# Performance work log

Measured on AMD Instinct MI355X. Metric: run time of the kernel, lower is better.

## Reference

```python
import jax, jax.numpy as jnp
import numpy as np

C = 256
CQK = C // 8  # query/key channels


def setup_inputs() -> dict:
    key = jax.random.key(0)
    ks = jax.random.split(key, 7)
    B, H, W = 4, 64, 64
    x = jax.random.normal(ks[0], (B, C, H, W), dtype=jnp.float32)
    # 1x1 conv weights stored as [out_ch, in_ch] (kernel spatial dims are 1)
    sc = 1.0 / np.sqrt(C)
    Wq = jax.random.uniform(ks[1], (CQK, C), jnp.float32, -sc, sc)
    bq = jax.random.uniform(ks[2], (CQK,), jnp.float32, -sc, sc)
    Wk = jax.random.uniform(ks[3], (CQK, C), jnp.float32, -sc, sc)
    bk = jax.random.uniform(ks[4], (CQK,), jnp.float32, -sc, sc)
    Wv = jax.random.uniform(ks[5], (C, C), jnp.float32, -sc, sc)
    bv = jax.random.uniform(ks[6], (C,), jnp.float32, -sc, sc)
    gamma = jnp.zeros((1,), dtype=jnp.float32)
    return {"x": x, "Wq": Wq, "bq": bq, "Wk": Wk, "bk": bk, "Wv": Wv, "bv": bv, "gamma": gamma}


def reference(x, Wq, bq, Wk, bk, Wv, bv, gamma):
    B, Ch, H, W = x.shape
    N = H * W
    xf = x.reshape(B, Ch, N)  # [B, C, N]
    # 1x1 convs == per-pixel linear projections
    q = jnp.einsum('oc,bcn->bno', Wq, xf) + bq  # [B, N, CQK]
    k = jnp.einsum('oc,bcn->bon', Wk, xf) + bk[None, :, None]  # [B, CQK, N]
    v = jnp.einsum('oc,bcn->bon', Wv, xf) + bv[None, :, None]  # [B, C, N]
    s = jnp.einsum('bnd,bdm->bnm', q, k)  # [B, N, N]
    attn = jax.nn.softmax(s, axis=-1)
    # out[b,c,i] = sum_j v[b,c,j] * attn[b,i,j]
    out = jnp.einsum('bcj,bij->bci', v, attn).reshape(B, Ch, H, W)
    return x + gamma[0] * out
```

## Files before the change

kernel.cpp:

```cpp
#include <hip/hip_runtime.h>
#include <math.h>

#define BATCH 4
#define CCH   256
#define DQK   32
#define NPIX  4096
#define LOG2E 1.44269504088896340736f

typedef __attribute__((ext_vector_type(8)))  short          short8_t;
typedef __attribute__((ext_vector_type(4)))  unsigned short ushort4_t;
typedef __attribute__((ext_vector_type(8)))  unsigned short ushort8_t;
typedef __attribute__((ext_vector_type(16))) float          f32x16;
typedef __attribute__((ext_vector_type(2)))  unsigned int   uint2_t;

#if __has_builtin(__builtin_amdgcn_exp2f)
#define EXP2F(x) __builtin_amdgcn_exp2f(x)
#else
#define EXP2F(x) exp2f(x)
#endif

#define MFMA32(a, b, c) __builtin_amdgcn_mfma_f32_32x32x16_bf16(a, b, c, 0, 0, 0)

static __device__ __forceinline__ unsigned short f2bf(float f) {
    union { float f; unsigned int u; } v; v.f = f;
    unsigned int r = v.u + 0x7FFFu + ((v.u >> 16) & 1u);
    return (unsigned short)(r >> 16);
}

static __device__ __forceinline__ short8_t cat8(ushort4_t a, ushort4_t b) {
    ushort8_t c = __builtin_shufflevector(a, b, 0, 1, 2, 3, 4, 5, 6, 7);
    short8_t r; __builtin_memcpy(&r, &c, 16); return r;
}

static __device__ __forceinline__ short8_t u4_to_s8(const unsigned int* u) {
    short8_t r; __builtin_memcpy(&r, u, 16); return r;
}

static __device__ __forceinline__ uint2_t plswap(unsigned int a, unsigned int b) {
#if __has_builtin(__builtin_amdgcn_permlane32_swap)
    return __builtin_amdgcn_permlane32_swap(a, b, false, false);
#else
    const unsigned int sa = (unsigned int)__shfl_xor((int)a, 32);
    const unsigned int sb = (unsigned int)__shfl_xor((int)b, 32);
    const int h = (threadIdx.x >> 5) & 1;
    uint2_t r;
    r.x = h ? sb : a;
    r.y = h ? b : sa;
    return r;
#endif
}

static __device__ __forceinline__ void make_bfrag(
    const f32x16& s, float& l0, float& l1, unsigned int bfr[2][4])
{
    float pv[16];
    #pragma unroll
    for (int r = 0; r < 16; ++r) pv[r] = EXP2F(s[r]);
    #pragma unroll
    for (int r = 0; r < 16; r += 2) { l0 += pv[r]; l1 += pv[r + 1]; }
    unsigned int P[8];
    #pragma unroll
    for (int v = 0; v < 8; ++v)
        P[v] = __builtin_amdgcn_perm(__float_as_uint(pv[2 * v + 1]),
                                     __float_as_uint(pv[2 * v]), 0x07060302u);
    #pragma unroll
    for (int kp = 0; kp < 2; ++kp) {
        const uint2_t r02 = plswap(P[4 * kp + 0], P[4 * kp + 2]);
        const uint2_t r13 = plswap(P[4 * kp + 1], P[4 * kp + 3]);
        bfr[kp][0] = r02.x; bfr[kp][1] = r13.x;
        bfr[kp][2] = r02.y; bfr[kp][3] = r13.y;
    }
}

__global__ __launch_bounds__(256) void wconv_kernel(
    const float* __restrict__ Wq, const float* __restrict__ Wk,
    const float* __restrict__ Wv, unsigned short* __restrict__ wbf)
{
    const int idx = blockIdx.x * 256 + threadIdx.x;
    const int o = idx >> 8, c = idx & 255;
    float v;
    if (o < 32)      v = Wq[o * 256 + c] * LOG2E;
    else if (o < 64) v = Wk[(o - 32) * 256 + c];
    else             v = Wv[(o - 64) * 256 + c];
    wbf[((c >> 3) * 320 + o) * 8 + (c & 7)] = f2bf(v);
}

__global__ __launch_bounds__(256) void xt_kernel(
    const float* __restrict__ x, unsigned short* __restrict__ xfrag)
{
    const int b  = blockIdx.x >> 6;
    const int cg = (blockIdx.x >> 4) & 3;
    const int ng = blockIdx.x & 15;
    const int t  = threadIdx.x;
    const int w = t >> 6, l = t & 63;

    #pragma unroll
    for (int sgl = 0; sgl < 2; ++sgl) {
        const int sg = w * 2 + sgl;
        float f[4][8];
        #pragma unroll
        for (int p = 0; p < 8; ++p) {
            const float* row = x + ((size_t)(b * CCH + cg * 64 + sg * 8 + p)) * NPIX
                                 + ng * 256;
            #pragma unroll
            for (int j = 0; j < 4; ++j)
                f[j][p] = row[j * 64 + l];
        }
        #pragma unroll
        for (int j = 0; j < 4; ++j) {
            unsigned int d[4];
            #pragma unroll
            for (int k = 0; k < 4; ++k)
                d[k] = __builtin_amdgcn_perm(__float_as_uint(f[j][2 * k + 1]),
                                             __float_as_uint(f[j][2 * k]), 0x07060302u);
            const int nt = ng * 8 + j * 2 + (l >> 5);
            unsigned short* dst = xfrag +
                ((((size_t)(b * 128 + nt) * 32) + cg * 8 + sg) * 32 + (l & 31)) * 8;
            *(short8_t*)dst = u4_to_s8(d);
        }
    }
}

__global__ __launch_bounds__(320) void proj_kernel(
    const unsigned short* __restrict__ xfrag, const unsigned short* __restrict__ wbf,
    const float* __restrict__ bq, const float* __restrict__ bk,
    const float* __restrict__ bv,
    unsigned short* __restrict__ qfrag, unsigned short* __restrict__ kfrag,
    unsigned short* __restrict__ vfrag)
{
    __shared__ unsigned short qkb[2 * 2 * 32 * 40];
    __shared__ unsigned short vbuf[4 * 64 * 72];

    const int b   = blockIdx.x >> 6;
    const int nt0 = (blockIdx.x & 63) << 1;
    const int t   = threadIdx.x;
    const int w = t >> 6, lane = t & 63, il = lane & 31, h = lane >> 5;

    float4 bA[4], bB[4];
    #pragma unroll
    for (int g = 0; g < 4; ++g) {
        if (w == 0) {
            bA[g] = *(const float4*)&bq[8 * g + 4 * h];
            bB[g] = *(const float4*)&bk[8 * g + 4 * h];
        } else {
            bA[g] = *(const float4*)&bv[(w - 1) * 64 + 8 * g + 4 * h];
            bB[g] = *(const float4*)&bv[(w - 1) * 64 + 32 + 8 * g + 4 * h];
        }
    }

    f32x16 acc[2][2];
    #pragma unroll
    for (int a = 0; a < 2; ++a)
        #pragma unroll
        for (int i = 0; i < 2; ++i)
            #pragma unroll
            for (int r = 0; r < 16; ++r) acc[a][i][r] = 0.f;

    const unsigned short* wp = wbf + ((size_t)(h * 320 + w * 64 + il)) * 8;
    const unsigned short* xp0 = xfrag + (((size_t)(b * 128 + nt0) * 32 + h) * 32 + il) * 8;
    const unsigned short* xp1 = xp0 + (size_t)32 * 32 * 8;

    #pragma unroll 4
    for (int ks = 0; ks < 16; ++ks) {
        const short8_t af0 = *(const short8_t*)(wp + ks * 5120);
        const short8_t af1 = *(const short8_t*)(wp + ks * 5120 + 256);
        const short8_t bf0 = *(const short8_t*)(xp0 + (size_t)ks * 2 * 256);
        const short8_t bf1 = *(const short8_t*)(xp1 + (size_t)ks * 2 * 256);
        acc[0][0] = MFMA32(af0, bf0, acc[0][0]);
        acc[0][1] = MFMA32(af0, bf1, acc[0][1]);
        acc[1][0] = MFMA32(af1, bf0, acc[1][0]);
        acc[1][1] = MFMA32(af1, bf1, acc[1][1]);
    }

    if (w == 0) {
        #pragma unroll
        for (int it = 0; it < 2; ++it)
            #pragma unroll
            for (int r = 0; r < 16; ++r) {
                const int d = (r & 3) + 8 * (r >> 2) + 4 * h;
                qkb[(it * 2 + 0) * 1280 + il * 40 + d] =
                    f2bf(acc[0][it][r] + bA[r >> 2][r & 3] * LOG2E);
                qkb[(it * 2 + 1) * 1280 + il * 40 + d] =
                    f2bf(acc[1][it][r] + bB[r >> 2][r & 3]);
            }
        #pragma unroll
        for (int it = 0; it < 2; ++it)
            #pragma unroll
            for (int rep = 0; rep < 2; ++rep) {
                const int u = rep * 64 + lane;
                const int slot = u >> 5, n = u & 31;
                ushort4_t qlo = *(const ushort4_t*)&qkb[(it * 2) * 1280 + n * 40 + slot * 8];
                ushort4_t qhi = *(const ushort4_t*)&qkb[(it * 2) * 1280 + n * 40 + slot * 8 + 4];
                ushort4_t klo = *(const ushort4_t*)&qkb[(it * 2 + 1) * 1280 + n * 40 + slot * 8];
                ushort4_t khi = *(const ushort4_t*)&qkb[(it * 2 + 1) * 1280 + n * 40 + slot * 8 + 4];
                const size_t o8 = (((size_t)(b * 128 + nt0 + it) * 4 + slot) * 32 + n) * 8;
                *(short8_t*)(qfrag + o8) = cat8(qlo, qhi);
                *(short8_t*)(kfrag + o8) = cat8(klo, khi);
            }
    } else {
        unsigned short* vb = vbuf + (w - 1) * 64 * 72;
        #pragma unroll
        for (int it = 0; it < 2; ++it)
            #pragma unroll
            for (int r = 0; r < 16; ++r) {
                const int orow = (r & 3) + 8 * (r >> 2) + 4 * h;
                vb[(orow)      * 72 + it * 32 + il] = f2bf(acc[0][it][r] + bA[r >> 2][r & 3]);
                vb[(orow + 32) * 72 + it * 32 + il] = f2bf(acc[1][it][r] + bB[r >> 2][r & 3]);
            }
        #pragma unroll
        for (int rep = 0; rep < 8; ++rep) {
            const int u = rep * 64 + lane;
            const int c = u & 63, m = u >> 6;
            const int it = m >> 2, slot = m & 3;
            ushort4_t lo = *(const ushort4_t*)&vb[c * 72 + it * 32 + slot * 8];
            ushort4_t hi = *(const ushort4_t*)&vb[c * 72 + it * 32 + slot * 8 + 4];
            const size_t o8 = (((size_t)(b * 128 + nt0 + it) * 4 + slot) * 256 +
                               (w - 1) * 64 + c) * 8;
            *(short8_t*)(vfrag + o8) = cat8(lo, hi);
        }
    }
}

struct KStage { short8_t k0, k1; };

__global__ __launch_bounds__(512) void attn_kernel(
    const unsigned short* __restrict__ qfrag,
    const unsigned short* __restrict__ kfrag,
    const unsigned short* __restrict__ vfrag,
    const float* __restrict__ x,
    const float* __restrict__ gamma,
    float* __restrict__ out)
{
    __shared__ float comb[8][64][17];

    const int m8 = blockIdx.x & 7;
    const int b  = m8 >> 1;
    const int itile = ((blockIdx.x >> 3) << 1) | (m8 & 1);
    const int i0 = itile << 6;
    const int t  = threadIdx.x;
    const int w = t >> 6, lane = t & 63, il = lane & 31, h = lane >> 5;
    const int ci = w & 1, jj = w >> 1;

    short8_t qf[2][2];
    #pragma unroll
    for (int it = 0; it < 2; ++it)
        #pragma unroll
        for (int ks = 0; ks < 2; ++ks)
            qf[it][ks] = *(const short8_t*)(qfrag +
                (((size_t)(b * 128 + itile * 2 + it) * 4 + ks * 2 + h) * 32 + il) * 8);

    const size_t kbase = (size_t)(b * 128 + jj * 32) * 1024 + h * 256 + il * 8;
    const size_t vbase = (size_t)(b * 128 + jj * 32) * 8192 + h * 2048 +
                         (ci * 128 + il) * 8;

    f32x16 zf;
    #pragma unroll
    for (int r = 0; r < 16; ++r) zf[r] = 0.f;
    f32x16 acc[2][4];
    #pragma unroll
    for (int a = 0; a < 2; ++a)
        #pragma unroll
        for (int c4 = 0; c4 < 4; ++c4) acc[a][c4] = zf;
    float ls[2][2] = {{0.f, 0.f}, {0.f, 0.f}};

    KStage A, B;
    short8_t v[4][2];

    auto loadK = [&](KStage& S, int jt) {
        const unsigned short* kp = kfrag + kbase + (size_t)jt * 1024;
        S.k0 = *(const short8_t*)kp;
        S.k1 = *(const short8_t*)(kp + 512);
    };
    auto loadV = [&](int jt) {
        const unsigned short* vp = vfrag + vbase + (size_t)jt * 8192;
        #pragma unroll
        for (int ct = 0; ct < 4; ++ct) {
            v[ct][0] = *(const short8_t*)(vp + ct * 256);
            v[ct][1] = *(const short8_t*)(vp + ct * 256 + 4096);
        }
    };
    auto step = [&](KStage& S, int kNext) {
        f32x16 s = MFMA32(S.k0, qf[0][0], zf);
        s = MFMA32(S.k1, qf[0][1], s);
        unsigned int bfr[2][4];
        make_bfrag(s, ls[0][0], ls[0][1], bfr);
        #pragma unroll
        for (int ct = 0; ct < 4; ++ct) {
            acc[0][ct] = MFMA32(v[ct][0], u4_to_s8(bfr[0]), acc[0][ct]);
            acc[0][ct] = MFMA32(v[ct][1], u4_to_s8(bfr[1]), acc[0][ct]);
        }
        s = MFMA32(S.k0, qf[1][0], zf);
        s = MFMA32(S.k1, qf[1][1], s);
        if (kNext < 32) loadK(S, kNext);
        make_bfrag(s, ls[1][0], ls[1][1], bfr);
        #pragma unroll
        for (int ct = 0; ct < 4; ++ct) {
            acc[1][ct] = MFMA32(v[ct][0], u4_to_s8(bfr[0]), acc[1][ct]);
            acc[1][ct] = MFMA32(v[ct][1], u4_to_s8(bfr[1]), acc[1][ct]);
        }
    };

    loadK(A, 0);
    loadK(B, 1);
    loadV(0);
    #pragma unroll 1
    for (int jt = 0; jt < 32; jt += 2) {
        step(A, jt + 2);
        loadV(jt + 1);
        step(B, jt + 3);
        if (jt + 2 < 32) loadV(jt + 2);
    }

    float l[2];
    #pragma unroll
    for (int it = 0; it < 2; ++it) {
        l[it] = ls[it][0] + ls[it][1];
        l[it] += __shfl_xor(l[it], 32);
    }
    const float gam = gamma[0];
    const int p1 = ci + 2 * ((jj + 1) & 3);
    const int p2 = ci + 2 * ((jj + 2) & 3);
    const int p3 = ci + 2 * ((jj + 3) & 3);
    float lt[2];

    #pragma unroll
    for (int it = 0; it < 2; ++it) {
        #pragma unroll 1
        for (int ct = 0; ct < 4; ++ct) {
            __syncthreads();
            #pragma unroll
            for (int r = 0; r < 16; ++r) comb[w][lane][r] = acc[it][ct][r];
            if (ct == 0) comb[w][lane][16] = l[it];
            __syncthreads();
            if (ct == 0)
                lt[it] = l[it] + comb[p1][lane][16] + comb[p2][lane][16] +
                         comb[p3][lane][16];
            if (jj == ct) {
                const float sc = gam / lt[it];
                #pragma unroll
                for (int r = 0; r < 16; ++r) {
                    const float o = acc[it][ct][r] + comb[p1][lane][r] +
                                    comb[p2][lane][r] + comb[p3][lane][r];
                    const int c = ci * 128 + ct * 32 + (r & 3) + 8 * (r >> 2) + 4 * h;
                    const size_t idx = ((size_t)(b * CCH + c)) * NPIX + i0 +
                                       it * 32 + il;
                    out[idx] = x[idx] + o * sc;
                }
            }
        }
    }
}

extern "C" void kernel_launch(void* const* d_in, const int* in_sizes, int n_in,
                              void* d_out, int out_size, void* d_ws, size_t ws_size,
                              hipStream_t stream) {
    const float* x     = (const float*)d_in[0];
    const float* Wq    = (const float*)d_in[1];
    const float* bq    = (const float*)d_in[2];
    const float* Wk    = (const float*)d_in[3];
    const float* bk    = (const float*)d_in[4];
    const float* Wv    = (const float*)d_in[5];
    const float* bv    = (const float*)d_in[6];
    const float* gamma = (const float*)d_in[7];
    float* out = (float*)d_out;

    unsigned short* ws    = (unsigned short*)d_ws;
    unsigned short* wbf   = ws;
    unsigned short* xfrag = ws + 81920;
    unsigned short* qfrag = xfrag + (size_t)4194304;
    unsigned short* kfrag = qfrag + (size_t)524288;
    unsigned short* vfrag = kfrag + (size_t)524288;

    wconv_kernel<<<dim3(320), dim3(256), 0, stream>>>(Wq, Wk, Wv, wbf);
    xt_kernel<<<dim3(256), dim3(256), 0, stream>>>(x, xfrag);
    proj_kernel<<<dim3(256), dim3(320), 0, stream>>>(
        xfrag, wbf, bq, bk, bv, qfrag, kfrag, vfrag);
    attn_kernel<<<dim3(256), dim3(512), 0, stream>>>(
        qfrag, kfrag, vfrag, x, gamma, out);
}
```

Measured before the change: 170.0 us.

## Repartition attention warps across query sub-tiles and halve the key split

Each of the 8 waves now owns one 32-row query sub-tile, one half of the channels, and one half of the key range (64 tiles), where before it handled both query sub-tiles over a quarter of the keys. This halves the per-wave accumulator registers, and launch bounds now request 2 blocks per SM for more occupancy. The cross-wave reduction shrinks from four partners to one. The trade-off is that each K/V fragment load now feeds one query sub-tile instead of two, so global/L2 traffic per block doubles and the per-wave loop is twice as long.

```diff
diff --git a/kernel.cpp b/kernel.cpp
--- a/kernel.cpp
+++ b/kernel.cpp
@@ -223,7 +223,7 @@
 
 struct KStage { short8_t k0, k1; };
 
-__global__ __launch_bounds__(512) void attn_kernel(
+__global__ __launch_bounds__(512, 2) void attn_kernel(
     const unsigned short* __restrict__ qfrag,
     const unsigned short* __restrict__ kfrag,
     const unsigned short* __restrict__ vfrag,
@@ -239,29 +239,25 @@
     const int i0 = itile << 6;
     const int t  = threadIdx.x;
     const int w = t >> 6, lane = t & 63, il = lane & 31, h = lane >> 5;
-    const int ci = w & 1, jj = w >> 1;
-
-    short8_t qf[2][2];
-    #pragma unroll
-    for (int it = 0; it < 2; ++it)
-        #pragma unroll
-        for (int ks = 0; ks < 2; ++ks)
-            qf[it][ks] = *(const short8_t*)(qfrag +
-                (((size_t)(b * 128 + itile * 2 + it) * 4 + ks * 2 + h) * 32 + il) * 8);
-
-    const size_t kbase = (size_t)(b * 128 + jj * 32) * 1024 + h * 256 + il * 8;
-    const size_t vbase = (size_t)(b * 128 + jj * 32) * 8192 + h * 2048 +
+    const int it = w & 1, ci = (w >> 1) & 1, jj = w >> 2;
+
+    short8_t qf[2];
+    #pragma unroll
+    for (int ks = 0; ks < 2; ++ks)
+        qf[ks] = *(const short8_t*)(qfrag +
+            (((size_t)(b * 128 + itile * 2 + it) * 4 + ks * 2 + h) * 32 + il) * 8);
+
+    const size_t kbase = (size_t)(b * 128 + jj * 64) * 1024 + h * 256 + il * 8;
+    const size_t vbase = (size_t)(b * 128 + jj * 64) * 8192 + h * 2048 +
                          (ci * 128 + il) * 8;
 
     f32x16 zf;
     #pragma unroll
     for (int r = 0; r < 16; ++r) zf[r] = 0.f;
-    f32x16 acc[2][4];
-    #pragma unroll
-    for (int a = 0; a < 2; ++a)
-        #pragma unroll
-        for (int c4 = 0; c4 < 4; ++c4) acc[a][c4] = zf;
-    float ls[2][2] = {{0.f, 0.f}, {0.f, 0.f}};
+    f32x16 acc[4];
+    #pragma unroll
+    for (int c4 = 0; c4 < 4; ++c4) acc[c4] = zf;
+    float ls[2] = {0.f, 0.f};
 
     KStage A, B;
     short8_t v[4][2];
@@ -280,23 +276,15 @@
         }
     };
     auto step = [&](KStage& S, int kNext) {
-        f32x16 s = MFMA32(S.k0, qf[0][0], zf);
-        s = MFMA32(S.k1, qf[0][1], s);
+        f32x16 s = MFMA32(S.k0, qf[0], zf);
+        s = MFMA32(S.k1, qf[1], s);
+        if (kNext < 64) loadK(S, kNext);
         unsigned int bfr[2][4];
-        make_bfrag(s, ls[0][0], ls[0][1], bfr);
+        make_bfrag(s, ls[0], ls[1], bfr);
         #pragma unroll
         for (int ct = 0; ct < 4; ++ct) {
-            acc[0][ct] = MFMA32(v[ct][0], u4_to_s8(bfr[0]), acc[0][ct]);
-            acc[0][ct] = MFMA32(v[ct][1], u4_to_s8(bfr[1]), acc[0][ct]);
-        }
-        s = MFMA32(S.k0, qf[1][0], zf);
-        s = MFMA32(S.k1, qf[1][1], s);
-        if (kNext < 32) loadK(S, kNext);
-        make_bfrag(s, ls[1][0], ls[1][1], bfr);
-        #pragma unroll
-        for (int ct = 0; ct < 4; ++ct) {
-            acc[1][ct] = MFMA32(v[ct][0], u4_to_s8(bfr[0]), acc[1][ct]);
-            acc[1][ct] = MFMA32(v[ct][1], u4_to_s8(bfr[1]), acc[1][ct]);
+            acc[ct] = MFMA32(v[ct][0], u4_to_s8(bfr[0]), acc[ct]);
+            acc[ct] = MFMA32(v[ct][1], u4_to_s8(bfr[1]), acc[ct]);
         }
     };
 
@@ -304,48 +292,36 @@
     loadK(B, 1);
     loadV(0);
     #pragma unroll 1
-    for (int jt = 0; jt < 32; jt += 2) {
+    for (int jt = 0; jt < 64; jt += 2) {
         step(A, jt + 2);
         loadV(jt + 1);
         step(B, jt + 3);
-        if (jt + 2 < 32) loadV(jt + 2);
-    }
-
-    float l[2];
-    #pragma unroll
-    for (int it = 0; it < 2; ++it) {
-        l[it] = ls[it][0] + ls[it][1];
-        l[it] += __shfl_xor(l[it], 32);
-    }
+        if (jt + 2 < 64) loadV(jt + 2);
+    }
+
+    float l = ls[0] + ls[1];
+    l += __shfl_xor(l, 32);
     const float gam = gamma[0];
-    const int p1 = ci + 2 * ((jj + 1) & 3);
-    const int p2 = ci + 2 * ((jj + 2) & 3);
-    const int p3 = ci + 2 * ((jj + 3) & 3);
-    float lt[2];
-
-    #pragma unroll
-    for (int it = 0; it < 2; ++it) {
-        #pragma unroll 1
-        for (int ct = 0; ct < 4; ++ct) {
-            __syncthreads();
-            #pragma unroll
-            for (int r = 0; r < 16; ++r) comb[w][lane][r] = acc[it][ct][r];
-            if (ct == 0) comb[w][lane][16] = l[it];
-            __syncthreads();
-            if (ct == 0)
-                lt[it] = l[it] + comb[p1][lane][16] + comb[p2][lane][16] +
-                         comb[p3][lane][16];
-            if (jj == ct) {
-                const float sc = gam / lt[it];
-                #pragma unroll
-                for (int r = 0; r < 16; ++r) {
-                    const float o = acc[it][ct][r] + comb[p1][lane][r] +
-                                    comb[p2][lane][r] + comb[p3][lane][r];
-                    const int c = ci * 128 + ct * 32 + (r & 3) + 8 * (r >> 2) + 4 * h;
-                    const size_t idx = ((size_t)(b * CCH + c)) * NPIX + i0 +
-                                       it * 32 + il;
-                    out[idx] = x[idx] + o * sc;
-                }
+    const int pw = w ^ 4;
+    float lt = 0.f;
+
+    #pragma unroll 1
+    for (int ct = 0; ct < 4; ++ct) {
+        __syncthreads();
+        #pragma unroll
+        for (int r = 0; r < 16; ++r) comb[w][lane][r] = acc[ct][r];
+        if (ct == 0) comb[w][lane][16] = l;
+        __syncthreads();
+        if (ct == 0) lt = l + comb[pw][lane][16];
+        if ((ct >> 1) == jj) {
+            const float sc = gam / lt;
+            #pragma unroll
+            for (int r = 0; r < 16; ++r) {
+                const float o = acc[ct][r] + comb[pw][lane][r];
+                const int c = ci * 128 + ct * 32 + (r & 3) + 8 * (r >> 2) + 4 * h;
+                const size_t idx = ((size_t)(b * CCH + c)) * NPIX + i0 +
+                                   it * 32 + il;
+                out[idx] = x[idx] + o * sc;
             }
         }
     }
```

New measurement: 160.6 us. 5.6% less time.
